# Optimization experiments

Hardware: AMD Instinct MI355X
Metric: run time of the kernel (lower is better)

Reference implementation:

```python
import jax, jax.numpy as jnp
import numpy as np

K = 20
EPS = 1e-5
NEG_SLOPE = 0.2


def knn(x, k):
    # x: [B, C, N] -> idx [B, N, k] of nearest neighbors (negative sq-dist topk)
    inner = -2.0 * jnp.einsum('bcn,bcm->bnm', x, x)
    xx = jnp.sum(x * x, axis=1)  # [B, N]
    d = -xx[:, :, None] - inner - xx[:, None, :]
    return jax.lax.top_k(d, k)[1]


def get_graph_feature(x, k):
    # x: [B, C, N] -> [B, 2C, N, k]
    idx = knn(x, k)
    xt = jnp.transpose(x, (0, 2, 1))            # [B, N, C]
    feat = jax.vmap(lambda a, i: a[i])(xt, idx)  # [B, N, k, C]
    center = xt[:, :, None, :]
    out = jnp.concatenate([feat - center, jnp.broadcast_to(center, feat.shape)], axis=-1)
    return jnp.transpose(out, (0, 3, 1, 2))


def conv_bn_lrelu(x, w, g, b):
    # 1x1 conv + BatchNorm2d (batch stats, training mode) + LeakyReLU(0.2)
    y = jnp.einsum('oc,bcnk->bonk', w, x)
    mu = jnp.mean(y, axis=(0, 2, 3), keepdims=True)
    var = jnp.mean((y - mu) ** 2, axis=(0, 2, 3), keepdims=True)
    y = (y - mu) * jax.lax.rsqrt(var + EPS)
    y = y * g[None, :, None, None] + b[None, :, None, None]
    return jnp.where(y >= 0, y, NEG_SLOPE * y)


def lrelu(y):
    return jnp.where(y >= 0, y, NEG_SLOPE * y)


def setup_inputs() -> dict:
    key = jax.random.key(0)
    ks = jax.random.split(key, 24)
    B, N = 8, 4096
    d = {}
    d['x'] = jax.random.normal(ks[0], (B, 3, N), dtype=jnp.float32)
    def wconv(k_, o, c):
        return jax.random.normal(k_, (o, c), dtype=jnp.float32) * (1.0 / np.sqrt(c))
    d['w1'] = wconv(ks[1], 32, 6)
    d['g1'] = 1.0 + 0.1 * jax.random.normal(ks[2], (32,), dtype=jnp.float32)
    d['b1'] = 0.1 * jax.random.normal(ks[3], (32,), dtype=jnp.float32)
    d['w2'] = wconv(ks[4], 64, 70)
    d['g2'] = 1.0 + 0.1 * jax.random.normal(ks[5], (64,), dtype=jnp.float32)
    d['b2'] = 0.1 * jax.random.normal(ks[6], (64,), dtype=jnp.float32)
    d['wd1'] = wconv(ks[7], 64, 64)
    d['gd1'] = 1.0 + 0.1 * jax.random.normal(ks[8], (64,), dtype=jnp.float32)
    d['bd1'] = 0.1 * jax.random.normal(ks[9], (64,), dtype=jnp.float32)
    d['wd2'] = wconv(ks[10], 64, 128)
    d['gd2'] = 1.0 + 0.1 * jax.random.normal(ks[11], (64,), dtype=jnp.float32)
    d['bd2'] = 0.1 * jax.random.normal(ks[12], (64,), dtype=jnp.float32)
    d['W2d'] = jax.random.normal(ks[13], (128, 128), dtype=jnp.float32) * (1.0 / np.sqrt(128))
    d['b2d'] = 0.1 * jax.random.normal(ks[14], (128,), dtype=jnp.float32)
    d['W3d'] = jax.random.normal(ks[15], (64, 128), dtype=jnp.float32) * (1.0 / np.sqrt(128))
    d['b3d'] = 0.1 * jax.random.normal(ks[16], (64,), dtype=jnp.float32)
    d['W4d'] = jax.random.normal(ks[17], (11, 64), dtype=jnp.float32) * (1.0 / np.sqrt(64))
    d['b4d'] = 0.1 * jax.random.normal(ks[18], (11,), dtype=jnp.float32)
    return d


def reference(x, w1, g1, b1, w2, g2, b2, wd1, gd1, bd1, wd2, gd2, bd2,
              W2d, b2d, W3d, b3d, W4d, b4d):
    x1_gf = get_graph_feature(x, K)                    # [B, 6, N, k]
    x1_max = jnp.max(conv_bn_lrelu(x1_gf, w1, g1, b1), axis=-1)  # [B, 32, N]
    x2_gf = jnp.concatenate([x1_gf, get_graph_feature(x1_max, K)], axis=1)  # [B, 70, N, k]
    x2_max = jnp.max(conv_bn_lrelu(x2_gf, w2, g2, b2), axis=-1)  # [B, 64, N]
    xd1 = jnp.max(conv_bn_lrelu(get_graph_feature(x1_max, K), wd1, gd1, bd1), axis=-1)  # [B, 64, N]
    xd2 = jnp.max(conv_bn_lrelu(get_graph_feature(x2_max, K), wd2, gd2, bd2), axis=-1)  # [B, 64, N]
    h = jnp.concatenate([xd1, xd2], axis=1)            # [B, 128, N]
    h = h.reshape(1, -1, 128)                          # faithful row-major view
    h = jnp.mean(h, axis=1)                            # [1, 128]
    h = lrelu(h @ W2d.T + b2d)
    h = lrelu(h @ W3d.T + b3d)
    return lrelu(h @ W4d.T + b4d)                      # [1, 11]
```

## Files before the change

kernel.cpp:

```cpp
#include <hip/hip_runtime.h>

#define BB 8
#define NN 4096
#define KK 20
constexpr float EPSV = 1e-5f;
constexpr float SLOPE = 0.2f;

typedef __bf16 bfrag __attribute__((ext_vector_type(8)));
typedef float floatx4 __attribute__((ext_vector_type(4)));
typedef unsigned short us4 __attribute__((ext_vector_type(4)));
typedef unsigned short us8 __attribute__((ext_vector_type(8)));

__device__ __forceinline__ float lrelu(float v) { return v >= 0.f ? v : SLOPE * v; }

__device__ __forceinline__ unsigned short bf16rn(float f) {
    unsigned int u = __float_as_uint(f);
    return (unsigned short)((u + 0x7FFFu + ((u >> 16) & 1u)) >> 16);
}
__device__ __forceinline__ float bf16up(unsigned short h) {
    return __uint_as_float(((unsigned int)h) << 16);
}

__device__ __forceinline__ void gl_lds16(const unsigned short* g, unsigned short* l) {
    __builtin_amdgcn_global_load_lds((const __attribute__((address_space(1))) void*)g,
                                     (__attribute__((address_space(3))) void*)l, 16, 0, 0);
}

__global__ void zero_kernel(float* p, int n) {
    int i = blockIdx.x * 256 + threadIdx.x;
    if (i < n) p[i] = 0.f;
}

template<int C>
__global__ void pack_kernel(const float* __restrict__ src, unsigned short* __restrict__ pk) {
    constexpr int SK = 2 * C + 8;
    const int id = blockIdx.x;
    const int b = id & 7;
    const int m0 = (id >> 3) * 64;
    const int tid = threadIdx.x;
    for (int i = tid; i < 64 * (C / 4); i += 256) {
        int m = i & 63;
        int c4 = (i >> 6) * 4;
        us4 hv, lv;
        #pragma unroll
        for (int j = 0; j < 4; j++) {
            float v = src[(b * C + c4 + j) * NN + m0 + m];
            unsigned short h = bf16rn(v);
            hv[j] = h;
            lv[j] = bf16rn(v - bf16up(h));
        }
        *(us4*)(&pk[(size_t)(b * NN + m0 + m) * SK + c4]) = hv;
        *(us4*)(&pk[(size_t)(b * NN + m0 + m) * SK + C + c4]) = lv;
    }
    if (tid < 64) {
        float s = 0.f;
        for (int c = 0; c < C; c++) {
            float v = src[(b * C + c) * NN + m0 + tid];
            s += v * v;
        }
        unsigned int ub = __float_as_uint(0.5f * s);
        us8 z;
        #pragma unroll
        for (int j = 0; j < 8; j++) z[j] = 0;
        z[0] = (unsigned short)(ub & 0xFFFFu);
        z[1] = (unsigned short)(ub >> 16);
        *(us8*)(&pk[(size_t)(b * NN + m0 + tid) * SK + 2 * C]) = z;
    }
}

__global__ void pack3_kernel(const float* __restrict__ src, unsigned short* __restrict__ pk) {
    const int id = blockIdx.x;
    const int b = id & 7;
    const int m = (id >> 3) * 256 + threadIdx.x;
    us8 w0, w1;
    #pragma unroll
    for (int j = 0; j < 8; j++) { w0[j] = 0; w1[j] = 0; }
    unsigned short row[12];
    float s = 0.f;
    #pragma unroll
    for (int c = 0; c < 3; c++) {
        float v = src[(b * 3 + c) * NN + m];
        s += v * v;
        unsigned short h = bf16rn(v);
        unsigned short l = bf16rn(v - bf16up(h));
        row[c] = h; row[3 + c] = l; row[6 + c] = l; row[9 + c] = h;
    }
    #pragma unroll
    for (int j = 0; j < 8; j++) w0[j] = row[j];
    #pragma unroll
    for (int j = 0; j < 4; j++) w1[j] = row[8 + j];
    unsigned short* dst = pk + (size_t)(b * NN + m) * 40;
    us8 z;
    #pragma unroll
    for (int j = 0; j < 8; j++) z[j] = 0;
    unsigned int ub = __float_as_uint(0.5f * s);
    us8 zh = z;
    zh[0] = (unsigned short)(ub & 0xFFFFu);
    zh[1] = (unsigned short)(ub >> 16);
    *(us8*)(dst) = w0;
    *(us8*)(dst + 8) = w1;
    *(us8*)(dst + 16) = z;
    *(us8*)(dst + 24) = z;
    *(us8*)(dst + 32) = zh;
}

template<int C>
__global__ __launch_bounds__(256) void knn_kernel(const float* __restrict__ src,
                                                  const unsigned short* __restrict__ pk,
                                                  int* __restrict__ idx) {
    constexpr int SK = (C == 3) ? 40 : (2 * C + 8);
    constexpr int HNOFF = (C == 3) ? 32 : 2 * C;
    constexpr int UNITS = 8 * SK;
    constexpr int PF = (UNITS + 255) / 256;
    constexpr int KKN = (C == 3) ? 1 : (C / 32);
    __shared__ __attribute__((aligned(16))) unsigned short cpack[2 * 64 * SK];
    __shared__ float pv[64 * 65];
    __shared__ unsigned short pidx[64 * 66];
    __shared__ float tau[64];
    __shared__ int cnt[64];
    __shared__ unsigned short qls[(C == 3) ? 64 * 40 : 2];

    const int bid = blockIdx.x;
    const int b = bid & 7;
    const int q0 = (bid >> 3) * 64;
    const int tid = threadIdx.x;
    const int lane = tid & 63;
    const int wv = tid >> 6;
    const int wr = (wv >> 1) * 32;
    const int wc = (wv & 1) * 32;
    const int fl = lane & 15;
    const int fq = lane >> 4;

    float tv[20]; int ti[20];
    #pragma unroll
    for (int k = 0; k < 20; k++) { tv[k] = -3.4e38f; ti[k] = 0; }

    bfrag qah[KKN][2], qal[KKN][2];
    if (C == 3) {
        for (int i = tid; i < 64 * 20; i += 256) {
            int r = i / 20, k = 12 + i % 20;
            qls[r * 40 + k] = 0;
        }
        if (tid < 64) {
            #pragma unroll
            for (int c = 0; c < 3; c++) {
                float v = src[(b * 3 + c) * NN + q0 + tid];
                unsigned short h = bf16rn(v);
                unsigned short l = bf16rn(v - bf16up(h));
                qls[tid * 40 + c] = h;  qls[tid * 40 + 3 + c] = l;
                qls[tid * 40 + 6 + c] = h;  qls[tid * 40 + 9 + c] = l;
            }
        }
    } else {
        #pragma unroll
        for (int r2 = 0; r2 < 2; r2++) {
            const unsigned short* qr = pk + (size_t)(b * NN + q0 + wr + r2 * 16 + fl) * SK + fq * 8;
            #pragma unroll
            for (int kk = 0; kk < KKN; kk++) {
                qah[kk][r2] = *(const bfrag*)(qr + kk * 32);
                qal[kk][r2] = *(const bfrag*)(qr + C + kk * 32);
            }
        }
    }

    {
        const unsigned short* p0 = pk + (size_t)(b * NN) * SK;
        #pragma unroll
        for (int r = 0; r < PF; r++) {
            int u0 = r * 256 + wv * 64;
            if (u0 < UNITS)
                gl_lds16(p0 + (size_t)(u0 + lane) * 8, cpack + (size_t)u0 * 8);
        }
    }
    if (tid < 64) { tau[tid] = -3.4e38f; cnt[tid] = 0; }
    __syncthreads();

    bfrag qa3[2];
    if (C == 3) {
        #pragma unroll
        for (int r2 = 0; r2 < 2; r2++)
            qa3[r2] = *(const bfrag*)(&qls[(wr + r2 * 16 + fl) * 40 + fq * 8]);
    }

    int buf = 0;
    for (int ch = 0; ch < 64; ch++) {
        unsigned short* cur = cpack + buf * (64 * SK);
        if (ch + 1 < 64) {
            unsigned short* nxt = cpack + (buf ^ 1) * (64 * SK);
            const unsigned short* pn = pk + (size_t)(b * NN + (ch + 1) * 64) * SK;
            #pragma unroll
            for (int r = 0; r < PF; r++) {
                int u0 = r * 256 + wv * 64;
                if (u0 < UNITS)
                    gl_lds16(pn + (size_t)(u0 + lane) * 8, nxt + (size_t)u0 * 8);
            }
        }

        floatx4 acc[2][2];
        #pragma unroll
        for (int r2 = 0; r2 < 2; r2++)
            #pragma unroll
            for (int c2 = 0; c2 < 2; c2++)
                acc[r2][c2] = (floatx4)(0.f);

        if (C == 3) {
            #pragma unroll
            for (int c2 = 0; c2 < 2; c2++) {
                bfrag bm = *(const bfrag*)(&cur[(wc + c2 * 16 + fl) * SK + fq * 8]);
                #pragma unroll
                for (int r2 = 0; r2 < 2; r2++)
                    acc[r2][c2] = __builtin_amdgcn_mfma_f32_16x16x32_bf16(qa3[r2], bm, acc[r2][c2], 0, 0, 0);
            }
        } else {
            #pragma unroll
            for (int kk = 0; kk < KKN; kk++) {
                const int kb = kk * 32 + fq * 8;
                bfrag bh[2], bl[2];
                #pragma unroll
                for (int c2 = 0; c2 < 2; c2++) {
                    bh[c2] = *(const bfrag*)(&cur[(wc + c2 * 16 + fl) * SK + kb]);
                    bl[c2] = *(const bfrag*)(&cur[(wc + c2 * 16 + fl) * SK + C + kb]);
                }
                #pragma unroll
                for (int r2 = 0; r2 < 2; r2++)
                    #pragma unroll
                    for (int c2 = 0; c2 < 2; c2++) {
                        acc[r2][c2] = __builtin_amdgcn_mfma_f32_16x16x32_bf16(qah[kk][r2], bh[c2], acc[r2][c2], 0, 0, 0);
                        acc[r2][c2] = __builtin_amdgcn_mfma_f32_16x16x32_bf16(qah[kk][r2], bl[c2], acc[r2][c2], 0, 0, 0);
                        acc[r2][c2] = __builtin_amdgcn_mfma_f32_16x16x32_bf16(qal[kk][r2], bh[c2], acc[r2][c2], 0, 0, 0);
                        acc[r2][c2] = __builtin_amdgcn_mfma_f32_16x16x32_bf16(qal[kk][r2], bl[c2], acc[r2][c2], 0, 0, 0);
                    }
            }
        }

        {
            const int m0 = ch * 64;
            float hvv[2];
            #pragma unroll
            for (int c2 = 0; c2 < 2; c2++)
                hvv[c2] = *(const float*)(&cur[(wc + c2 * 16 + fl) * SK + HNOFF]);
            #pragma unroll
            for (int r2 = 0; r2 < 2; r2++) {
                const int qb = wr + r2 * 16 + fq * 4;
                float4 t4 = *(const float4*)(&tau[qb]);
                float ta[4] = { t4.x, t4.y, t4.z, t4.w };
                #pragma unroll
                for (int c2 = 0; c2 < 2; c2++) {
                    const float hv = hvv[c2];
                    const int mm = m0 + wc + c2 * 16 + fl;
                    #pragma unroll
                    for (int reg = 0; reg < 4; reg++) {
                        float s = acc[r2][c2][reg] - hv;
                        if (s > ta[reg]) {
                            int q = qb + reg;
                            int p = atomicAdd(&cnt[q], 1);
                            pv[q * 65 + p] = s;
                            pidx[q * 66 + p] = (unsigned short)mm;
                        }
                    }
                }
            }
        }
        __syncthreads();

        if (tid < 64) {
            int n = cnt[tid];
            for (int t = 0; t < n; t++) {
                float v = pv[tid * 65 + t];
                if (v > tv[0]) {
                    tv[0] = v; ti[0] = (int)pidx[tid * 66 + t];
                    #pragma unroll
                    for (int j = 0; j < 19; j++) {
                        if (tv[j] > tv[j + 1]) {
                            float a = tv[j]; tv[j] = tv[j + 1]; tv[j + 1] = a;
                            int bi = ti[j]; ti[j] = ti[j + 1]; ti[j + 1] = bi;
                        }
                    }
                }
            }
            cnt[tid] = 0;
            tau[tid] = tv[0];
        }
        __syncthreads();
        buf ^= 1;
    }

    if (tid < 64) {
        #pragma unroll
        for (int k = 0; k < 20; k++)
            idx[(b * NN + q0 + tid) * KK + k] = ti[k];
    }
}

template<int COUT>
__global__ void precompute_kernel(const float* __restrict__ src, int C,
                                  const float* __restrict__ w, int CIN, int wd_off, int wc_off,
                                  float* __restrict__ G, float* __restrict__ H) {
    constexpr int MY = 256 / COUT;
    extern __shared__ float lds[];
    float* wd = lds;
    float* wc = lds + C * COUT;
    const int id = blockIdx.x;
    const int b = id & 7;
    const int m_base = (id >> 3) * 64;
    const int tid = threadIdx.y * COUT + threadIdx.x;
    for (int i = tid; i < C * COUT; i += 256) {
        int c = i / COUT, o = i % COUT;
        float a  = w[o * CIN + wd_off + c];
        float cc = w[o * CIN + wc_off + c];
        wd[i] = a;
        wc[i] = cc - a;
    }
    __syncthreads();
    const int o = threadIdx.x;
    for (int it = 0; it < COUT / 4; it++) {
        int m = m_base + it * MY + threadIdx.y;
        float g = 0.f, h = 0.f;
        for (int c = 0; c < C; c++) {
            float s = src[(b * C + c) * NN + m];
            g += wd[c * COUT + o] * s;
            h += wc[c * COUT + o] * s;
        }
        int gi = (b * NN + m) * COUT + o;
        G[gi] = g;
        H[gi] = h;
    }
}

__global__ void precompute2_kernel(const float* __restrict__ srcA, const float* __restrict__ srcB,
                                   const float* __restrict__ w,
                                   float* __restrict__ GA, float* __restrict__ GB,
                                   float* __restrict__ H) {
    constexpr int COUT = 64, CA = 3, CB = 32, CIN = 70;
    __shared__ float wdA[CA * COUT], wcA[CA * COUT], wdB[CB * COUT], wcB[CB * COUT];
    const int id = blockIdx.x;
    const int b = id & 7;
    const int m_base = (id >> 3) * 64;
    const int tid = threadIdx.y * COUT + threadIdx.x;
    for (int i = tid; i < CA * COUT; i += 256) {
        int c = i / COUT, o = i % COUT;
        float a = w[o * CIN + 0 + c], cc = w[o * CIN + 3 + c];
        wdA[i] = a; wcA[i] = cc - a;
    }
    for (int i = tid; i < CB * COUT; i += 256) {
        int c = i / COUT, o = i % COUT;
        float a = w[o * CIN + 6 + c], cc = w[o * CIN + 38 + c];
        wdB[i] = a; wcB[i] = cc - a;
    }
    __syncthreads();
    const int o = threadIdx.x;
    for (int it = 0; it < 16; it++) {
        int m = m_base + it * 4 + threadIdx.y;
        float ga = 0.f, gb = 0.f, h = 0.f;
        for (int c = 0; c < CA; c++) {
            float s = srcA[(b * CA + c) * NN + m];
            ga += wdA[c * COUT + o] * s;
            h  += wcA[c * COUT + o] * s;
        }
        for (int c = 0; c < CB; c++) {
            float s = srcB[(b * CB + c) * NN + m];
            gb += wdB[c * COUT + o] * s;
            h  += wcB[c * COUT + o] * s;
        }
        int gi = (b * NN + m) * COUT + o;
        GA[gi] = ga;
        GB[gi] = gb;
        H[gi] = h;
    }
}

template<int COUT, int GROUPS>
__global__ void conv_stats_kernel(const float* __restrict__ G1, const int* __restrict__ idx1,
                                  const float* __restrict__ G2, const int* __restrict__ idx2,
                                  const float* __restrict__ H, const float* __restrict__ gw,
                                  float* __restrict__ stats, float* __restrict__ V) {
    constexpr int NY = 256 / COUT;
    const int id = blockIdx.x;
    const int b = id & 7;
    const int o = threadIdx.x;
    const int n = (id >> 3) * NY + threadIdx.y;
    const int base = b * NN + n;
    const float h = H[base * COUT + o];
    float s1 = 0.f, s2 = 0.f;
    float gx = -3.4e38f, gn = 3.4e38f;
    #pragma unroll
    for (int k = 0; k < KK; k++) {
        int i1 = idx1[base * KK + k];
        float g = G1[(b * NN + i1) * COUT + o];
        if (GROUPS == 2) {
            int i2 = idx2[base * KK + k];
            g += G2[(b * NN + i2) * COUT + o];
        }
        float y = g + h;
        s1 += y;
        s2 += y * y;
        gx = fmaxf(gx, g);
        gn = fminf(gn, g);
    }
    V[base * COUT + o] = ((gw[o] >= 0.f) ? gx : gn) + h;

    __shared__ float ls[2 * COUT];
    if (threadIdx.y == 0) { ls[o] = 0.f; ls[COUT + o] = 0.f; }
    __syncthreads();
    atomicAdd(&ls[o], s1);
    atomicAdd(&ls[COUT + o], s2);
    __syncthreads();
    if (threadIdx.y == 0) {
        atomicAdd(&stats[o], ls[o]);
        atomicAdd(&stats[64 + o], ls[COUT + o]);
    }
}

__global__ void apply_kernel(const float* __restrict__ V, const float* __restrict__ stats,
                             const float* __restrict__ g, const float* __restrict__ bb,
                             float* __restrict__ out, int cout, float invP) {
    const int id = blockIdx.x;
    const int b = id & 7;
    int e = (id >> 3) * 256 + threadIdx.x;
    int n = e & (NN - 1);
    int o = e >> 12;
    __shared__ float sc_s, sh_s;
    if (threadIdx.x == 0) {
        float mu  = stats[o] * invP;
        float var = stats[64 + o] * invP - mu * mu;
        float sc  = g[o] * rsqrtf(var + EPSV);
        sc_s = sc;
        sh_s = bb[o] - mu * sc;
    }
    __syncthreads();
    float v = V[(b * NN + n) * cout + o];
    out[(b * cout + o) * NN + n] = lrelu(sc_s * v + sh_s);
}

__global__ void mean_kernel(const float* __restrict__ xd1, const float* __restrict__ xd2,
                            float* __restrict__ hsum) {
    __shared__ float bins[128];
    const int tid = threadIdx.x;
    if (tid < 128) bins[tid] = 0.f;
    __syncthreads();
    const int half = BB * 64 * NN;
    const int stride = gridDim.x * 256;
    for (int e = blockIdx.x * 256 + tid; e < half; e += stride)
        atomicAdd(&bins[e & 127], xd1[e]);
    for (int e = blockIdx.x * 256 + tid; e < half; e += stride)
        atomicAdd(&bins[e & 127], xd2[e]);
    __syncthreads();
    if (tid < 128) atomicAdd(&hsum[tid], bins[tid]);
}

__global__ void head_kernel(const float* __restrict__ hsum,
                            const float* __restrict__ W2d, const float* __restrict__ b2d,
                            const float* __restrict__ W3d, const float* __restrict__ b3d,
                            const float* __restrict__ W4d, const float* __restrict__ b4d,
                            float* __restrict__ out) {
    __shared__ float h[128], t1[128], t2[64];
    const int t = threadIdx.x;
    h[t] = hsum[t] * (1.f / 32768.f);
    __syncthreads();
    float a = b2d[t];
    for (int j = 0; j < 128; j++) a += W2d[t * 128 + j] * h[j];
    t1[t] = lrelu(a);
    __syncthreads();
    if (t < 64) {
        float a2 = b3d[t];
        for (int j = 0; j < 128; j++) a2 += W3d[t * 128 + j] * t1[j];
        t2[t] = lrelu(a2);
    }
    __syncthreads();
    if (t < 11) {
        float a3 = b4d[t];
        for (int j = 0; j < 64; j++) a3 += W4d[t * 64 + j] * t2[j];
        out[t] = lrelu(a3);
    }
}

extern "C" void kernel_launch(void* const* d_in, const int* in_sizes, int n_in,
                              void* d_out, int out_size, void* d_ws, size_t ws_size,
                              hipStream_t stream) {
    const float* x   = (const float*)d_in[0];
    const float* w1  = (const float*)d_in[1];
    const float* g1  = (const float*)d_in[2];
    const float* b1  = (const float*)d_in[3];
    const float* w2  = (const float*)d_in[4];
    const float* g2  = (const float*)d_in[5];
    const float* b2  = (const float*)d_in[6];
    const float* wd1 = (const float*)d_in[7];
    const float* gd1 = (const float*)d_in[8];
    const float* bd1 = (const float*)d_in[9];
    const float* wd2 = (const float*)d_in[10];
    const float* gd2 = (const float*)d_in[11];
    const float* bd2 = (const float*)d_in[12];
    const float* W2d = (const float*)d_in[13];
    const float* b2d = (const float*)d_in[14];
    const float* W3d = (const float*)d_in[15];
    const float* b3d = (const float*)d_in[16];
    const float* W4d = (const float*)d_in[17];
    const float* b4d = (const float*)d_in[18];
    float* out = (float*)d_out;

    char* ws = (char*)d_ws;
    size_t off = 0;
    auto alloc = [&](size_t bytes) { char* p = ws + off; off += (bytes + 255) & ~size_t(255); return p; };
    int*   idx1  = (int*)  alloc(BB * NN * KK * 4);
    int*   idx2  = (int*)  alloc(BB * NN * KK * 4);
    int*   idx3  = (int*)  alloc(BB * NN * KK * 4);
    float* x1m   = (float*)alloc(BB * 32 * NN * 4);
    float* x2m   = (float*)alloc(BB * 64 * NN * 4);
    float* xd1   = (float*)alloc(BB * 64 * NN * 4);
    float* xd2   = (float*)alloc(BB * 64 * NN * 4);
    float* G1    = (float*)alloc((size_t)BB * NN * 64 * 4);
    float* G2    = (float*)alloc((size_t)BB * NN * 64 * 4);
    float* H     = (float*)alloc((size_t)BB * NN * 64 * 4);
    float* Vbuf  = (float*)alloc((size_t)BB * NN * 64 * 4);
    float* pad   = (float*)alloc((size_t)BB * NN * 64 * 4);
    float* stats = (float*)alloc(4 * 256 * 4);
    float* hsum  = (float*)alloc(128 * 4);
    (void)pad;

    float* st0 = stats;
    float* st1 = stats + 256;
    float* st2 = stats + 512;
    float* st3 = stats + 768;

    unsigned short* pkbuf = (unsigned short*)Vbuf;

    const float invP = 1.f / (float)(BB * NN * KK);
    const dim3 knn_grid(NN / 64 * BB);
    const dim3 pre_grid(NN / 64 * BB);

    zero_kernel<<<5, 256, 0, stream>>>(stats, 1024 + 128);

    pack3_kernel<<<NN / 256 * BB, 256, 0, stream>>>(x, pkbuf);
    knn_kernel<3><<<knn_grid, 256, 0, stream>>>(x, pkbuf, idx1);

    precompute_kernel<32><<<pre_grid, dim3(32, 8), 2 * 3 * 32 * 4, stream>>>(
        x, 3, w1, 6, 0, 3, G1, H);
    conv_stats_kernel<32, 1><<<NN / 8 * BB, dim3(32, 8), 0, stream>>>(
        G1, idx1, nullptr, nullptr, H, g1, st0, Vbuf);
    apply_kernel<<<32 * NN / 256 * BB, 256, 0, stream>>>(Vbuf, st0, g1, b1, x1m, 32, invP);

    pack_kernel<32><<<pre_grid, 256, 0, stream>>>(x1m, pkbuf);
    knn_kernel<32><<<knn_grid, 256, 0, stream>>>(x1m, pkbuf, idx2);

    precompute2_kernel<<<pre_grid, dim3(64, 4), 0, stream>>>(x, x1m, w2, G1, G2, H);
    conv_stats_kernel<64, 2><<<NN / 4 * BB, dim3(64, 4), 0, stream>>>(
        G1, idx1, G2, idx2, H, g2, st1, Vbuf);
    apply_kernel<<<64 * NN / 256 * BB, 256, 0, stream>>>(Vbuf, st1, g2, b2, x2m, 64, invP);

    precompute_kernel<64><<<pre_grid, dim3(64, 4), 2 * 32 * 64 * 4, stream>>>(
        x1m, 32, wd1, 64, 0, 32, G2, H);
    conv_stats_kernel<64, 1><<<NN / 4 * BB, dim3(64, 4), 0, stream>>>(
        G2, idx2, nullptr, nullptr, H, gd1, st2, Vbuf);
    apply_kernel<<<64 * NN / 256 * BB, 256, 0, stream>>>(Vbuf, st2, gd1, bd1, xd1, 64, invP);

    pack_kernel<64><<<pre_grid, 256, 0, stream>>>(x2m, pkbuf);
    knn_kernel<64><<<knn_grid, 256, 0, stream>>>(x2m, pkbuf, idx3);

    precompute_kernel<64><<<pre_grid, dim3(64, 4), 2 * 64 * 64 * 4, stream>>>(
        x2m, 64, wd2, 128, 0, 64, G2, H);
    conv_stats_kernel<64, 1><<<NN / 4 * BB, dim3(64, 4), 0, stream>>>(
        G2, idx3, nullptr, nullptr, H, gd2, st3, Vbuf);
    apply_kernel<<<64 * NN / 256 * BB, 256, 0, stream>>>(Vbuf, st3, gd2, bd2, xd2, 64, invP);

    mean_kernel<<<1024, 256, 0, stream>>>(xd1, xd2, hsum);
    head_kernel<<<1, 128, 0, stream>>>(hsum, W2d, b2d, W3d, b3d, W4d, b4d, out);
}
```

Baseline: 1.641 ms.

## Fuse precompute work into kNN launches as independent block roles

Result: slower. 2.203 ms (+34.3%).

```diff
diff --git a/kernel.cpp b/kernel.cpp
--- a/kernel.cpp
+++ b/kernel.cpp
@@ -104,10 +104,16 @@
     *(us8*)(dst + 32) = zh;
 }
 
-template<int C>
-__global__ __launch_bounds__(256) void knn_kernel(const float* __restrict__ src,
-                                                  const unsigned short* __restrict__ pk,
-                                                  int* __restrict__ idx) {
+template<int C, int PREMODE>
+__global__ __launch_bounds__(256) void knn_fused(const float* __restrict__ src,
+                                                 const unsigned short* __restrict__ pk,
+                                                 int* __restrict__ idx,
+                                                 const float* __restrict__ preA,
+                                                 const float* __restrict__ preB,
+                                                 const float* __restrict__ w,
+                                                 float* __restrict__ GA,
+                                                 float* __restrict__ GB,
+                                                 float* __restrict__ Hout) {
     constexpr int SK = (C == 3) ? 40 : (2 * C + 8);
     constexpr int HNOFF = (C == 3) ? 32 : 2 * C;
     constexpr int UNITS = 8 * SK;
@@ -122,8 +128,99 @@
 
     const int bid = blockIdx.x;
     const int b = bid & 7;
-    const int q0 = (bid >> 3) * 64;
+    const int group = bid >> 3;
+    const int role = group & 1;
+    const int sub = group >> 1;
     const int tid = threadIdx.x;
+
+    if (role == 1) {
+        const int m_base = sub * 64;
+        float* lw = (float*)cpack;
+        if constexpr (PREMODE == 1) {
+            constexpr int COUT = 32, CI = 3, CIN = 6;
+            float* wd = lw; float* wc = lw + CI * COUT;
+            for (int i = tid; i < CI * COUT; i += 256) {
+                int c = i / COUT, o = i % COUT;
+                float a = w[o * CIN + c], cc = w[o * CIN + 3 + c];
+                wd[i] = a; wc[i] = cc - a;
+            }
+            __syncthreads();
+            const int o = tid & 31, ty = tid >> 5;
+            for (int it = 0; it < 8; it++) {
+                int m = m_base + it * 8 + ty;
+                float g = 0.f, h = 0.f;
+                for (int c = 0; c < CI; c++) {
+                    float s = preA[(b * CI + c) * NN + m];
+                    g += wd[c * COUT + o] * s;
+                    h += wc[c * COUT + o] * s;
+                }
+                int gi = (b * NN + m) * COUT + o;
+                GA[gi] = g;
+                Hout[gi] = h;
+            }
+        } else if constexpr (PREMODE == 2) {
+            constexpr int COUT = 64, CA = 3, CB = 32, CIN = 70;
+            float* wdA = lw;
+            float* wcA = lw + 192;
+            float* wdB = lw + 384;
+            float* wcB = lw + 2432;
+            for (int i = tid; i < CA * COUT; i += 256) {
+                int c = i / COUT, o = i % COUT;
+                float a = w[o * CIN + 0 + c], cc = w[o * CIN + 3 + c];
+                wdA[i] = a; wcA[i] = cc - a;
+            }
+            for (int i = tid; i < CB * COUT; i += 256) {
+                int c = i / COUT, o = i % COUT;
+                float a = w[o * CIN + 6 + c], cc = w[o * CIN + 38 + c];
+                wdB[i] = a; wcB[i] = cc - a;
+            }
+            __syncthreads();
+            const int o = tid & 63, ty = tid >> 6;
+            for (int it = 0; it < 16; it++) {
+                int m = m_base + it * 4 + ty;
+                float ga = 0.f, gb = 0.f, h = 0.f;
+                for (int c = 0; c < CA; c++) {
+                    float s = preA[(b * CA + c) * NN + m];
+                    ga += wdA[c * COUT + o] * s;
+                    h  += wcA[c * COUT + o] * s;
+                }
+                for (int c = 0; c < CB; c++) {
+                    float s = preB[(b * CB + c) * NN + m];
+                    gb += wdB[c * COUT + o] * s;
+                    h  += wcB[c * COUT + o] * s;
+                }
+                int gi = (b * NN + m) * COUT + o;
+                GA[gi] = ga;
+                GB[gi] = gb;
+                Hout[gi] = h;
+            }
+        } else {
+            constexpr int COUT = 64, CI = 32, CIN = 64;
+            float* wd = lw; float* wc = lw + CI * COUT;
+            for (int i = tid; i < CI * COUT; i += 256) {
+                int c = i / COUT, o = i % COUT;
+                float a = w[o * CIN + c], cc = w[o * CIN + 32 + c];
+                wd[i] = a; wc[i] = cc - a;
+            }
+            __syncthreads();
+            const int o = tid & 63, ty = tid >> 6;
+            for (int it = 0; it < 16; it++) {
+                int m = m_base + it * 4 + ty;
+                float g = 0.f, h = 0.f;
+                for (int c = 0; c < CI; c++) {
+                    float s = preA[(b * CI + c) * NN + m];
+                    g += wd[c * COUT + o] * s;
+                    h += wc[c * COUT + o] * s;
+                }
+                int gi = (b * NN + m) * COUT + o;
+                GA[gi] = g;
+                Hout[gi] = h;
+            }
+        }
+        return;
+    }
+
+    const int q0 = sub * 64;
     const int lane = tid & 63;
     const int wv = tid >> 6;
     const int wr = (wv >> 1) * 32;
@@ -323,48 +420,6 @@
         }
         int gi = (b * NN + m) * COUT + o;
         G[gi] = g;
-        H[gi] = h;
-    }
-}
-
-__global__ void precompute2_kernel(const float* __restrict__ srcA, const float* __restrict__ srcB,
-                                   const float* __restrict__ w,
-                                   float* __restrict__ GA, float* __restrict__ GB,
-                                   float* __restrict__ H) {
-    constexpr int COUT = 64, CA = 3, CB = 32, CIN = 70;
-    __shared__ float wdA[CA * COUT], wcA[CA * COUT], wdB[CB * COUT], wcB[CB * COUT];
-    const int id = blockIdx.x;
-    const int b = id & 7;
-    const int m_base = (id >> 3) * 64;
-    const int tid = threadIdx.y * COUT + threadIdx.x;
-    for (int i = tid; i < CA * COUT; i += 256) {
-        int c = i / COUT, o = i % COUT;
-        float a = w[o * CIN + 0 + c], cc = w[o * CIN + 3 + c];
-        wdA[i] = a; wcA[i] = cc - a;
-    }
-    for (int i = tid; i < CB * COUT; i += 256) {
-        int c = i / COUT, o = i % COUT;
-        float a = w[o * CIN + 6 + c], cc = w[o * CIN + 38 + c];
-        wdB[i] = a; wcB[i] = cc - a;
-    }
-    __syncthreads();
-    const int o = threadIdx.x;
-    for (int it = 0; it < 16; it++) {
-        int m = m_base + it * 4 + threadIdx.y;
-        float ga = 0.f, gb = 0.f, h = 0.f;
-        for (int c = 0; c < CA; c++) {
-            float s = srcA[(b * CA + c) * NN + m];
-            ga += wdA[c * COUT + o] * s;
-            h  += wcA[c * COUT + o] * s;
-        }
-        for (int c = 0; c < CB; c++) {
-            float s = srcB[(b * CB + c) * NN + m];
-            gb += wdB[c * COUT + o] * s;
-            h  += wcB[c * COUT + o] * s;
-        }
-        int gi = (b * NN + m) * COUT + o;
-        GA[gi] = ga;
-        GB[gi] = gb;
         H[gi] = h;
     }
 }
@@ -525,41 +580,39 @@
     unsigned short* pkbuf = (unsigned short*)Vbuf;
 
     const float invP = 1.f / (float)(BB * NN * KK);
-    const dim3 knn_grid(NN / 64 * BB);
+    const dim3 fused_grid(2 * NN / 64 * BB);
     const dim3 pre_grid(NN / 64 * BB);
 
     zero_kernel<<<5, 256, 0, stream>>>(stats, 1024 + 128);
 
     pack3_kernel<<<NN / 256 * BB, 256, 0, stream>>>(x, pkbuf);
-    knn_kernel<3><<<knn_grid, 256, 0, stream>>>(x, pkbuf, idx1);
-
-    precompute_kernel<32><<<pre_grid, dim3(32, 8), 2 * 3 * 32 * 4, stream>>>(
-        x, 3, w1, 6, 0, 3, G1, H);
+    knn_fused<3, 1><<<fused_grid, 256, 0, stream>>>(x, pkbuf, idx1,
+        x, nullptr, w1, G1, nullptr, H);
+
     conv_stats_kernel<32, 1><<<NN / 8 * BB, dim3(32, 8), 0, stream>>>(
         G1, idx1, nullptr, nullptr, H, g1, st0, Vbuf);
     apply_kernel<<<32 * NN / 256 * BB, 256, 0, stream>>>(Vbuf, st0, g1, b1, x1m, 32, invP);
 
     pack_kernel<32><<<pre_grid, 256, 0, stream>>>(x1m, pkbuf);
-    knn_kernel<32><<<knn_grid, 256, 0, stream>>>(x1m, pkbuf, idx2);
-
-    precompute2_kernel<<<pre_grid, dim3(64, 4), 0, stream>>>(x, x1m, w2, G1, G2, H);
+    knn_fused<32, 2><<<fused_grid, 256, 0, stream>>>(x1m, pkbuf, idx2,
+        x, x1m, w2, G1, G2, H);
+
     conv_stats_kernel<64, 2><<<NN / 4 * BB, dim3(64, 4), 0, stream>>>(
         G1, idx1, G2, idx2, H, g2, st1, Vbuf);
     apply_kernel<<<64 * NN / 256 * BB, 256, 0, stream>>>(Vbuf, st1, g2, b2, x2m, 64, invP);
 
-    precompute_kernel<64><<<pre_grid, dim3(64, 4), 2 * 32 * 64 * 4, stream>>>(
-        x1m, 32, wd1, 64, 0, 32, G2, H);
+    pack_kernel<64><<<pre_grid, 256, 0, stream>>>(x2m, pkbuf);
+    knn_fused<64, 3><<<fused_grid, 256, 0, stream>>>(x2m, pkbuf, idx3,
+        x1m, nullptr, wd1, G2, nullptr, H);
+
     conv_stats_kernel<64, 1><<<NN / 4 * BB, dim3(64, 4), 0, stream>>>(
         G2, idx2, nullptr, nullptr, H, gd1, st2, Vbuf);
     apply_kernel<<<64 * NN / 256 * BB, 256, 0, stream>>>(Vbuf, st2, gd1, bd1, xd1, 64, invP);
 
-    pack_kernel<64><<<pre_grid, 256, 0, stream>>>(x2m, pkbuf);
-    knn_kernel<64><<<knn_grid, 256, 0, stream>>>(x2m, pkbuf, idx3);
-
     precompute_kernel<64><<<pre_grid, dim3(64, 4), 2 * 64 * 64 * 4, stream>>>(
-        x2m, 64, wd2, 128, 0, 64, G2, H);
+        x2m, 64, wd2, 128, 0, 64, G1, H);
     conv_stats_kernel<64, 1><<<NN / 4 * BB, dim3(64, 4), 0, stream>>>(
-        G2, idx3, nullptr, nullptr, H, gd2, st3, Vbuf);
+        G1, idx3, nullptr, nullptr, H, gd2, st3, Vbuf);
     apply_kernel<<<64 * NN / 256 * BB, 256, 0, stream>>>(Vbuf, st3, gd2, bd2, xd2, 64, invP);
 
     mean_kernel<<<1024, 256, 0, stream>>>(xd1, xd2, hsum);
```
